# Kernel optimization log

Measured on AMD Instinct MI355X. Metric: run time of the kernel, lower is better.

The kernel has to match this reference:

```python
import jax, jax.numpy as jnp
import numpy as np

B = 8192      # batch
C = 4096      # in_channels
K = 5         # group_size (odd, centered window)


def setup_inputs() -> dict:
    key = jax.random.key(0)
    kx, kw, kb = jax.random.split(key, 3)
    x = jax.random.normal(kx, (B, C), dtype=jnp.float32)
    # Banded weights: W[i, k] multiplies x[:, i + k - K//2] (zero outside range).
    W = jax.random.normal(kw, (C, K), dtype=jnp.float32) * 0.1
    b = jax.random.normal(kb, (C,), dtype=jnp.float32) * 0.1
    return {"x": x, "W": W, "b": b}


def reference(x, W, b):
    # out[:, i] = sum_k W[i, k] * x[:, i + k - K//2] + b[i]
    # Boundary clipping in the original == zero padding here.
    Bn, Cn = x.shape
    Kn = W.shape[1]
    half = Kn // 2
    xp = jnp.pad(x, ((0, 0), (half, half)))  # [B, C + K - 1]
    acc = jnp.zeros_like(x)
    for k in range(Kn):  # tiny fixed loop (K=5), fused shift-multiply-add
        acc = acc + xp[:, k:k + Cn] * W[:, k]
    return acc + b
```

## Files before the change

### kernel.cpp

```cpp
#include <hip/hip_runtime.h>


#define B_ROWS 8192
#define C_CH   4096
#define KWIN   5
#define ROWS_PER_BLOCK 16

__global__ __launch_bounds__(256) void grouped_linear_kernel(
    const float* __restrict__ x, const float* __restrict__ W,
    const float* __restrict__ bias, float* __restrict__ out)
{
    const int chunk = (blockIdx.x << 8) + threadIdx.x;
    const int c     = chunk << 2;
    const int r0    = blockIdx.y * ROWS_PER_BLOCK;

    const float4* W4 = (const float4*)(W + (size_t)c * KWIN);
    const float4 w0 = W4[0];
    const float4 w1 = W4[1];
    const float4 w2 = W4[2];
    const float4 w3 = W4[3];
    const float4 w4 = W4[4];
    const float4 bv = ((const float4*)bias)[chunk];

    const bool has_m = (c > 0);
    const bool has_p = (c + 4 < C_CH);
    const float4 zero = make_float4(0.f, 0.f, 0.f, 0.f);

    const float4* xrow = (const float4*)(x   + (size_t)r0 * C_CH);
    float4*       orow = (float4*)      (out + (size_t)r0 * C_CH);

    #pragma unroll 2
    for (int r = 0; r < ROWS_PER_BLOCK; ++r) {
        const float4 xm = has_m ? xrow[chunk - 1] : zero;
        const float4 xc = xrow[chunk];
        const float4 xp = has_p ? xrow[chunk + 1] : zero;

        const float win0 = xm.z, win1 = xm.w;
        const float win2 = xc.x, win3 = xc.y, win4 = xc.z, win5 = xc.w;
        const float win6 = xp.x, win7 = xp.y;

        float4 o;
        o.x = fmaf(w0.x, win0, fmaf(w0.y, win1, fmaf(w0.z, win2, fmaf(w0.w, win3, fmaf(w1.x, win4, bv.x)))));
        o.y = fmaf(w1.y, win1, fmaf(w1.z, win2, fmaf(w1.w, win3, fmaf(w2.x, win4, fmaf(w2.y, win5, bv.y)))));
        o.z = fmaf(w2.z, win2, fmaf(w2.w, win3, fmaf(w3.x, win4, fmaf(w3.y, win5, fmaf(w3.z, win6, bv.z)))));
        o.w = fmaf(w3.w, win3, fmaf(w4.x, win4, fmaf(w4.y, win5, fmaf(w4.z, win6, fmaf(w4.w, win7, bv.w)))));

        orow[chunk] = o;
        xrow += C_CH / 4;
        orow += C_CH / 4;
    }
}

extern "C" void kernel_launch(void* const* d_in, const int* in_sizes, int n_in,
                              void* d_out, int out_size, void* d_ws, size_t ws_size,
                              hipStream_t stream) {
    const float* x    = (const float*)d_in[0];
    const float* W    = (const float*)d_in[1];
    const float* bias = (const float*)d_in[2];
    float* out = (float*)d_out;

    dim3 grid(C_CH / 4 / 256, B_ROWS / ROWS_PER_BLOCK);
    dim3 block(256);
    grouped_linear_kernel<<<grid, block, 0, stream>>>(x, W, bias, out);
}
```

Baseline: 249.6 us.

## Stage input rows into LDS via direct global-to-LDS loads with halo exchange

Rows of x are loaded once into shared memory using the global_load_lds builtin, with a small halo of two floats on each side loaded separately. Neighbour windows are then read from LDS instead of re-reading overlapping float4s from global memory. Rows per block drop from 16 to 4 and an occupancy hint is added to increase the number of resident blocks. This adds a barrier and LDS traffic per block, and relies on the wave-uniform LDS destination semantics of the builtin.

```diff
diff --git a/kernel.cpp b/kernel.cpp
--- a/kernel.cpp
+++ b/kernel.cpp
@@ -3,18 +3,26 @@
 
 #define B_ROWS 8192
 #define C_CH   4096
-#define KWIN   5
-#define ROWS_PER_BLOCK 16
+#define ROWS   4
+#define NCHK   256
 
-__global__ __launch_bounds__(256) void grouped_linear_kernel(
+typedef unsigned int u32;
+
+__global__ __launch_bounds__(256, 8) void grouped_linear_kernel(
     const float* __restrict__ x, const float* __restrict__ W,
     const float* __restrict__ bias, float* __restrict__ out)
 {
-    const int chunk = (blockIdx.x << 8) + threadIdx.x;
+    __shared__ __align__(16) float lds_rows[ROWS][1024];
+    __shared__ __align__(16) float lds_haloL[ROWS][4];
+    __shared__ __align__(16) float lds_haloR[ROWS][4];
+
+    const int tid   = threadIdx.x;
+    const int bx    = blockIdx.x;
+    const int r0    = blockIdx.y * ROWS;
+    const int chunk = bx * NCHK + tid;
     const int c     = chunk << 2;
-    const int r0    = blockIdx.y * ROWS_PER_BLOCK;
 
-    const float4* W4 = (const float4*)(W + (size_t)c * KWIN);
+    const float4* W4 = (const float4*)(W + (size_t)c * 5);
     const float4 w0 = W4[0];
     const float4 w1 = W4[1];
     const float4 w2 = W4[2];
@@ -22,22 +30,50 @@
     const float4 w4 = W4[4];
     const float4 bv = ((const float4*)bias)[chunk];
 
-    const bool has_m = (c > 0);
-    const bool has_p = (c + 4 < C_CH);
-    const float4 zero = make_float4(0.f, 0.f, 0.f, 0.f);
+    {
+        const int wave = tid >> 6;
+        const float* gsrc0 = x + (size_t)r0 * C_CH + bx * 1024 + tid * 4;
+        #pragma unroll
+        for (int r = 0; r < ROWS; ++r) {
+            const float* gsrc = gsrc0 + r * C_CH;
+            float* ldst = &lds_rows[r][wave * 256];
+            __builtin_amdgcn_global_load_lds(
+                (const __attribute__((address_space(1))) u32*)gsrc,
+                (__attribute__((address_space(3))) u32*)ldst,
+                16, 0, 0);
+        }
+    }
 
-    const float4* xrow = (const float4*)(x   + (size_t)r0 * C_CH);
-    float4*       orow = (float4*)      (out + (size_t)r0 * C_CH);
+    if (tid < 2 * ROWS) {
+        const int  hr    = tid >> 1;
+        const int  right = tid & 1;
+        const int  gc    = bx * 1024 + (right ? 1024 : -2);
+        float2 v = make_float2(0.f, 0.f);
+        if (gc >= 0 && gc + 1 < C_CH)
+            v = *(const float2*)(x + (size_t)(r0 + hr) * C_CH + gc);
+        float* dst = right ? &lds_haloR[hr][0] : &lds_haloL[hr][2];
+        *(float2*)dst = v;
+    }
 
-    #pragma unroll 2
-    for (int r = 0; r < ROWS_PER_BLOCK; ++r) {
-        const float4 xm = has_m ? xrow[chunk - 1] : zero;
-        const float4 xc = xrow[chunk];
-        const float4 xp = has_p ? xrow[chunk + 1] : zero;
+    __syncthreads();
 
-        const float win0 = xm.z, win1 = xm.w;
-        const float win2 = xc.x, win3 = xc.y, win4 = xc.z, win5 = xc.w;
-        const float win6 = xp.x, win7 = xp.y;
+    float4* obase = (float4*)(out + (size_t)r0 * C_CH) + chunk;
+    const int f = tid * 4;
+
+    #pragma unroll
+    for (int r = 0; r < ROWS; ++r) {
+        const float* rowp = lds_rows[r];
+        const float4 pm = (tid > 0)
+            ? *(const float4*)(rowp + f - 4)
+            : *(const float4*)lds_haloL[r];
+        const float4 pc = *(const float4*)(rowp + f);
+        const float4 pp = (tid < NCHK - 1)
+            ? *(const float4*)(rowp + f + 4)
+            : *(const float4*)lds_haloR[r];
+
+        const float win0 = pm.z, win1 = pm.w;
+        const float win2 = pc.x, win3 = pc.y, win4 = pc.z, win5 = pc.w;
+        const float win6 = pp.x, win7 = pp.y;
 
         float4 o;
         o.x = fmaf(w0.x, win0, fmaf(w0.y, win1, fmaf(w0.z, win2, fmaf(w0.w, win3, fmaf(w1.x, win4, bv.x)))));
@@ -45,9 +81,7 @@
         o.z = fmaf(w2.z, win2, fmaf(w2.w, win3, fmaf(w3.x, win4, fmaf(w3.y, win5, fmaf(w3.z, win6, bv.z)))));
         o.w = fmaf(w3.w, win3, fmaf(w4.x, win4, fmaf(w4.y, win5, fmaf(w4.z, win6, fmaf(w4.w, win7, bv.w)))));
 
-        orow[chunk] = o;
-        xrow += C_CH / 4;
-        orow += C_CH / 4;
+        obase[r * (C_CH / 4)] = o;
     }
 }
 
@@ -59,7 +93,7 @@
     const float* bias = (const float*)d_in[2];
     float* out = (float*)d_out;
 
-    dim3 grid(C_CH / 4 / 256, B_ROWS / ROWS_PER_BLOCK);
+    dim3 grid(C_CH / 1024, B_ROWS / ROWS);
     dim3 block(256);
     grouped_linear_kernel<<<grid, block, 0, stream>>>(x, W, bias, out);
 }
```

New measurement: 227.5 us. 1.1x faster.

## Stage input rows into LDS with async double-buffered global_load_lds and halos

Applied to the files above, without the earlier changes.

Rewrites the banded stencil so each block copies tiles of two rows into LDS using the asynchronous global-to-LDS load builtin, double-buffered across four row pairs. Neighbouring taps are read from LDS, plus small halo entries loaded separately at the tile edges, instead of three overlapping float4 global loads per thread. The aim is to overlap the next tile's loads with the current compute and to cut redundant global traffic on this memory-bound kernel. It adds barriers, LDS usage and an occupancy hint, and it depends on the async LDS loads having completed before each barrier.

```diff
diff --git a/kernel.cpp b/kernel.cpp
--- a/kernel.cpp
+++ b/kernel.cpp
@@ -3,18 +3,27 @@
 
 #define B_ROWS 8192
 #define C_CH   4096
-#define KWIN   5
-#define ROWS_PER_BLOCK 16
+#define TROWS  2
+#define NT     4
+#define NCHK   256
 
-__global__ __launch_bounds__(256) void grouped_linear_kernel(
+typedef unsigned int u32;
+
+__global__ __launch_bounds__(256, 8) void grouped_linear_kernel(
     const float* __restrict__ x, const float* __restrict__ W,
     const float* __restrict__ bias, float* __restrict__ out)
 {
-    const int chunk = (blockIdx.x << 8) + threadIdx.x;
+    __shared__ __align__(16) float lds_rows[2][TROWS][1024];
+    __shared__ __align__(16) float lds_hL[2][TROWS][4];
+    __shared__ __align__(16) float lds_hR[2][TROWS][4];
+
+    const int tid   = threadIdx.x;
+    const int bx    = blockIdx.x;
+    const int r0    = blockIdx.y * (TROWS * NT);
+    const int chunk = bx * NCHK + tid;
     const int c     = chunk << 2;
-    const int r0    = blockIdx.y * ROWS_PER_BLOCK;
 
-    const float4* W4 = (const float4*)(W + (size_t)c * KWIN);
+    const float4* W4 = (const float4*)(W + (size_t)c * 5);
     const float4 w0 = W4[0];
     const float4 w1 = W4[1];
     const float4 w2 = W4[2];
@@ -22,32 +31,79 @@
     const float4 w4 = W4[4];
     const float4 bv = ((const float4*)bias)[chunk];
 
-    const bool has_m = (c > 0);
-    const bool has_p = (c + 4 < C_CH);
-    const float4 zero = make_float4(0.f, 0.f, 0.f, 0.f);
+    const int wave = tid >> 6;
+    const float* gbase = x + (size_t)r0 * C_CH + bx * 1024 + tid * 4;
+    float4* obase = (float4*)(out + (size_t)r0 * C_CH) + chunk;
 
-    const float4* xrow = (const float4*)(x   + (size_t)r0 * C_CH);
-    float4*       orow = (float4*)      (out + (size_t)r0 * C_CH);
+    const int  hr     = tid >> 1;
+    const int  hside  = tid & 1;
+    const int  hgc    = bx * 1024 + (hside ? 1024 : -2);
+    const bool hvalid = (tid < 2 * TROWS) && (hgc >= 0) && (hgc + 1 < C_CH);
+    const float* hbase = x + (size_t)(r0 + hr) * C_CH + hgc;
 
-    #pragma unroll 2
-    for (int r = 0; r < ROWS_PER_BLOCK; ++r) {
-        const float4 xm = has_m ? xrow[chunk - 1] : zero;
-        const float4 xc = xrow[chunk];
-        const float4 xp = has_p ? xrow[chunk + 1] : zero;
+#define STAGE(buf_, t_) {                                                      \
+    const float* g_ = gbase + (size_t)(t_) * TROWS * C_CH;                     \
+    _Pragma("unroll")                                                          \
+    for (int r_ = 0; r_ < TROWS; ++r_)                                         \
+        __builtin_amdgcn_global_load_lds(                                      \
+            (const __attribute__((address_space(1))) u32*)(g_ + r_ * C_CH),    \
+            (__attribute__((address_space(3))) u32*)&lds_rows[buf_][r_][wave * 256], \
+            16, 0, 0);                                                         \
+  }
 
-        const float win0 = xm.z, win1 = xm.w;
-        const float win2 = xc.x, win3 = xc.y, win4 = xc.z, win5 = xc.w;
-        const float win6 = xp.x, win7 = xp.y;
+#define HLOAD(t_) {                                                            \
+    hv = make_float2(0.f, 0.f);                                                \
+    if (hvalid) hv = *(const float2*)(hbase + (size_t)(t_) * TROWS * C_CH);    \
+  }
 
-        float4 o;
-        o.x = fmaf(w0.x, win0, fmaf(w0.y, win1, fmaf(w0.z, win2, fmaf(w0.w, win3, fmaf(w1.x, win4, bv.x)))));
-        o.y = fmaf(w1.y, win1, fmaf(w1.z, win2, fmaf(w1.w, win3, fmaf(w2.x, win4, fmaf(w2.y, win5, bv.y)))));
-        o.z = fmaf(w2.z, win2, fmaf(w2.w, win3, fmaf(w3.x, win4, fmaf(w3.y, win5, fmaf(w3.z, win6, bv.z)))));
-        o.w = fmaf(w3.w, win3, fmaf(w4.x, win4, fmaf(w4.y, win5, fmaf(w4.z, win6, fmaf(w4.w, win7, bv.w)))));
+#define HWRITE(buf_) {                                                         \
+    if (tid < 2 * TROWS) {                                                     \
+        float* d_ = hside ? &lds_hR[buf_][hr][0] : &lds_hL[buf_][hr][2];       \
+        *(float2*)d_ = hv;                                                     \
+    }                                                                          \
+  }
 
-        orow[chunk] = o;
-        xrow += C_CH / 4;
-        orow += C_CH / 4;
+#define COMPUTE(buf_, t_) {                                                    \
+    _Pragma("unroll")                                                          \
+    for (int r_ = 0; r_ < TROWS; ++r_) {                                       \
+        const float* rowp = lds_rows[buf_][r_];                                \
+        const int f = tid * 4;                                                 \
+        const float4 pm = (tid > 0) ? *(const float4*)(rowp + f - 4)           \
+                                    : *(const float4*)lds_hL[buf_][r_];        \
+        const float4 pc = *(const float4*)(rowp + f);                          \
+        const float4 pp = (tid < NCHK - 1) ? *(const float4*)(rowp + f + 4)    \
+                                           : *(const float4*)lds_hR[buf_][r_]; \
+        const float win0 = pm.z, win1 = pm.w;                                  \
+        const float win2 = pc.x, win3 = pc.y, win4 = pc.z, win5 = pc.w;        \
+        const float win6 = pp.x, win7 = pp.y;                                  \
+        float4 o;                                                              \
+        o.x = fmaf(w0.x, win0, fmaf(w0.y, win1, fmaf(w0.z, win2, fmaf(w0.w, win3, fmaf(w1.x, win4, bv.x))))); \
+        o.y = fmaf(w1.y, win1, fmaf(w1.z, win2, fmaf(w1.w, win3, fmaf(w2.x, win4, fmaf(w2.y, win5, bv.y))))); \
+        o.z = fmaf(w2.z, win2, fmaf(w2.w, win3, fmaf(w3.x, win4, fmaf(w3.y, win5, fmaf(w3.z, win6, bv.z))))); \
+        o.w = fmaf(w3.w, win3, fmaf(w4.x, win4, fmaf(w4.y, win5, fmaf(w4.z, win6, fmaf(w4.w, win7, bv.w))))); \
+        obase[((t_) * TROWS + r_) * (C_CH / 4)] = o;                           \
+    }                                                                          \
+  }
+
+    float2 hv;
+
+    STAGE(0, 0);
+    HLOAD(0);
+    HWRITE(0);
+    __syncthreads();
+
+    #pragma unroll
+    for (int t = 0; t < NT; ++t) {
+        const int cur = t & 1;
+        if (t + 1 < NT) {
+            STAGE(cur ^ 1, t + 1);
+            HLOAD(t + 1);
+        }
+        COMPUTE(cur, t);
+        if (t + 1 < NT) {
+            HWRITE(cur ^ 1);
+            __syncthreads();
+        }
     }
 }
 
@@ -59,7 +115,7 @@
     const float* bias = (const float*)d_in[2];
     float* out = (float*)d_out;
 
-    dim3 grid(C_CH / 4 / 256, B_ROWS / ROWS_PER_BLOCK);
+    dim3 grid(C_CH / 1024, B_ROWS / (TROWS * NT));
     dim3 block(256);
     grouped_linear_kernel<<<grid, block, 0, stream>>>(x, W, bias, out);
 }
```

Result: faster. 237.0 us (-5.0%).

## Stage full rows into LDS with async triple-buffered global_load_lds pipeline

Applied to the files above, without the earlier changes.

Each block now owns a full row range of 8 rows and keeps the weights and bias for all 4096 channels in registers. Rows are streamed into a three-deep LDS ring with asynchronous global_load_lds, and explicit vmcnt waits plus barriers let the next rows load while the current row is computed. Neighbouring window values come from LDS instead of overlapping global loads. The cost is more registers, 48KB of LDS per block and hand-tuned waitcnt logic that depends on how loads and stores are counted.

```diff
diff --git a/kernel.cpp b/kernel.cpp
--- a/kernel.cpp
+++ b/kernel.cpp
@@ -3,51 +3,86 @@
 
 #define B_ROWS 8192
 #define C_CH   4096
-#define KWIN   5
-#define ROWS_PER_BLOCK 16
+#define NT     8
+#define NBUF   3
 
-__global__ __launch_bounds__(256) void grouped_linear_kernel(
+typedef unsigned int u32;
+
+__global__ __launch_bounds__(256, 3) void grouped_linear_kernel(
     const float* __restrict__ x, const float* __restrict__ W,
     const float* __restrict__ bias, float* __restrict__ out)
 {
-    const int chunk = (blockIdx.x << 8) + threadIdx.x;
-    const int c     = chunk << 2;
-    const int r0    = blockIdx.y * ROWS_PER_BLOCK;
+    __shared__ __align__(16) float lds[NBUF][C_CH];
 
-    const float4* W4 = (const float4*)(W + (size_t)c * KWIN);
-    const float4 w0 = W4[0];
-    const float4 w1 = W4[1];
-    const float4 w2 = W4[2];
-    const float4 w3 = W4[3];
-    const float4 w4 = W4[4];
-    const float4 bv = ((const float4*)bias)[chunk];
+    const int tid  = threadIdx.x;
+    const int wave = tid >> 6;
+    const int lane = tid & 63;
+    const int r0   = blockIdx.x * NT;
 
-    const bool has_m = (c > 0);
-    const bool has_p = (c + 4 < C_CH);
-    const float4 zero = make_float4(0.f, 0.f, 0.f, 0.f);
+    float4 w0[4], w1[4], w2[4], w3[4], w4[4], bv[4];
+    #pragma unroll
+    for (int q = 0; q < 4; ++q) {
+        const int chunk = q * 256 + tid;
+        const float4* W4p = (const float4*)(W + (size_t)chunk * 20);
+        w0[q] = W4p[0];
+        w1[q] = W4p[1];
+        w2[q] = W4p[2];
+        w3[q] = W4p[3];
+        w4[q] = W4p[4];
+        bv[q] = ((const float4*)bias)[chunk];
+    }
 
-    const float4* xrow = (const float4*)(x   + (size_t)r0 * C_CH);
-    float4*       orow = (float4*)      (out + (size_t)r0 * C_CH);
+    const float* xw = x + (size_t)r0 * C_CH + wave * 1024 + lane * 4;
 
-    #pragma unroll 2
-    for (int r = 0; r < ROWS_PER_BLOCK; ++r) {
-        const float4 xm = has_m ? xrow[chunk - 1] : zero;
-        const float4 xc = xrow[chunk];
-        const float4 xp = has_p ? xrow[chunk + 1] : zero;
+#define STAGE(t_) {                                                            \
+    const float* g_ = xw + (size_t)(t_) * C_CH;                                \
+    float* d_ = &lds[(t_) % NBUF][wave * 1024];                                \
+    _Pragma("unroll")                                                          \
+    for (int i_ = 0; i_ < 4; ++i_)                                             \
+        __builtin_amdgcn_global_load_lds(                                      \
+            (const __attribute__((address_space(1))) u32*)(g_ + i_ * 256),     \
+            (__attribute__((address_space(3))) u32*)(d_ + i_ * 256),           \
+            16, 0, 0);                                                         \
+  }
 
-        const float win0 = xm.z, win1 = xm.w;
-        const float win2 = xc.x, win3 = xc.y, win4 = xc.z, win5 = xc.w;
-        const float win6 = xp.x, win7 = xp.y;
+    STAGE(0);
+    STAGE(1);
 
-        float4 o;
-        o.x = fmaf(w0.x, win0, fmaf(w0.y, win1, fmaf(w0.z, win2, fmaf(w0.w, win3, fmaf(w1.x, win4, bv.x)))));
-        o.y = fmaf(w1.y, win1, fmaf(w1.z, win2, fmaf(w1.w, win3, fmaf(w2.x, win4, fmaf(w2.y, win5, bv.y)))));
-        o.z = fmaf(w2.z, win2, fmaf(w2.w, win3, fmaf(w3.x, win4, fmaf(w3.y, win5, fmaf(w3.z, win6, bv.z)))));
-        o.w = fmaf(w3.w, win3, fmaf(w4.x, win4, fmaf(w4.y, win5, fmaf(w4.z, win6, fmaf(w4.w, win7, bv.w)))));
+    #pragma unroll
+    for (int t = 0; t < NT; ++t) {
+        if (t == 0 || t == NT - 1) {
+            asm volatile("s_waitcnt vmcnt(4)" ::: "memory");
+        } else {
+            asm volatile("s_waitcnt vmcnt(8)" ::: "memory");
+        }
+        __builtin_amdgcn_s_barrier();
 
-        orow[chunk] = o;
-        xrow += C_CH / 4;
-        orow += C_CH / 4;
+        const float* row = lds[t % NBUF];
+        float4* orow = (float4*)(out + (size_t)(r0 + t) * C_CH);
+
+        #pragma unroll
+        for (int q = 0; q < 4; ++q) {
+            const int chunk = q * 256 + tid;
+            const int f = chunk * 4;
+            const float4 pm = *(const float4*)(row + (chunk > 0    ? f - 4 : 0));
+            const float4 pc = *(const float4*)(row + f);
+            const float4 pp = *(const float4*)(row + (chunk < 1023 ? f + 4 : f));
+            const bool lo = (chunk == 0), hi = (chunk == 1023);
+
+            const float win0 = lo ? 0.f : pm.z, win1 = lo ? 0.f : pm.w;
+            const float win2 = pc.x, win3 = pc.y, win4 = pc.z, win5 = pc.w;
+            const float win6 = hi ? 0.f : pp.x, win7 = hi ? 0.f : pp.y;
+
+            float4 o;
+            o.x = fmaf(w0[q].x, win0, fmaf(w0[q].y, win1, fmaf(w0[q].z, win2, fmaf(w0[q].w, win3, fmaf(w1[q].x, win4, bv[q].x)))));
+            o.y = fmaf(w1[q].y, win1, fmaf(w1[q].z, win2, fmaf(w1[q].w, win3, fmaf(w2[q].x, win4, fmaf(w2[q].y, win5, bv[q].y)))));
+            o.z = fmaf(w2[q].z, win2, fmaf(w2[q].w, win3, fmaf(w3[q].x, win4, fmaf(w3[q].y, win5, fmaf(w3[q].z, win6, bv[q].z)))));
+            o.w = fmaf(w3[q].w, win3, fmaf(w4[q].x, win4, fmaf(w4[q].y, win5, fmaf(w4[q].z, win6, fmaf(w4[q].w, win7, bv[q].w)))));
+
+            orow[chunk] = o;
+        }
+
+        if (t + 2 < NT) STAGE(t + 2);
     }
 }
 
@@ -59,7 +94,7 @@
     const float* bias = (const float*)d_in[2];
     float* out = (float*)d_out;
 
-    dim3 grid(C_CH / 4 / 256, B_ROWS / ROWS_PER_BLOCK);
+    dim3 grid(B_ROWS / NT);
     dim3 block(256);
     grouped_linear_kernel<<<grid, block, 0, stream>>>(x, W, bias, out);
 }
```

Result: faster. 243.9 us (-2.3%).
